# Optimization experiments

Measured on AMD Instinct MI355X. Metric: run time of the kernel, lower is better.

Reference implementation:

```python
import jax, jax.numpy as jnp
import numpy as np

N = 20000
IN_CH = 2048      # 64 * (768/24)
HID = 512
LAT = 128
KW = 24           # conv1d kernel == stride
COUT = 64
NEG_SLOPE = 0.2
BN_EPS = 1e-5


def gatv2(x, src, dst, Wl, bl, Wr, br, att, bias, n_nodes):
    # GATv2Conv (PyG semantics, 1 head): e_ij = att . leaky_relu(Wl x_j + Wr x_i)
    xl = x @ Wl + bl                      # [N, out] source-side features
    xr = x @ Wr + br                      # [N, out] target-side features
    e = jax.nn.leaky_relu(xl[src] + xr[dst], NEG_SLOPE) @ att   # [E]
    m = jax.ops.segment_max(e, dst, num_segments=n_nodes)       # per-target max
    a = jnp.exp(e - m[dst])
    s = jax.ops.segment_sum(a, dst, num_segments=n_nodes)
    alpha = a / (s[dst] + 1e-16)
    out = jax.ops.segment_sum(xl[src] * alpha[:, None], dst, num_segments=n_nodes)
    return out + bias


def setup_inputs() -> dict:
    key = jax.random.key(0)
    ks = jax.random.split(key, 16)
    x = jax.random.normal(ks[0], (N, 24, 32), dtype=jnp.float32)
    edge_index = jax.random.randint(ks[1], (2, 320000), 0, N, dtype=jnp.int32)
    sc = 0.02
    return {
        "x": x,
        "edge_index": edge_index,
        "conv_w": jax.random.normal(ks[2], (COUT, KW), dtype=jnp.float32) * sc,
        "conv_b": jnp.zeros((COUT,), dtype=jnp.float32),
        "W1l": jax.random.normal(ks[3], (IN_CH, HID), dtype=jnp.float32) * sc,
        "b1l": jnp.zeros((HID,), dtype=jnp.float32),
        "W1r": jax.random.normal(ks[4], (IN_CH, HID), dtype=jnp.float32) * sc,
        "b1r": jnp.zeros((HID,), dtype=jnp.float32),
        "att1": jax.random.normal(ks[5], (HID,), dtype=jnp.float32) * sc,
        "bias1": jnp.zeros((HID,), dtype=jnp.float32),
        "gamma": jnp.ones((HID,), dtype=jnp.float32),
        "beta": jnp.zeros((HID,), dtype=jnp.float32),
        "W2l": jax.random.normal(ks[6], (HID, LAT), dtype=jnp.float32) * sc,
        "b2l": jnp.zeros((LAT,), dtype=jnp.float32),
        "W2r": jax.random.normal(ks[7], (HID, LAT), dtype=jnp.float32) * sc,
        "b2r": jnp.zeros((LAT,), dtype=jnp.float32),
        "att2": jax.random.normal(ks[8], (LAT,), dtype=jnp.float32) * sc,
        "bias2": jnp.zeros((LAT,), dtype=jnp.float32),
    }


def reference(x, edge_index, conv_w, conv_b, W1l, b1l, W1r, b1r, att1, bias1,
              gamma, beta, W2l, b2l, W2r, b2r, att2, bias2):
    n = x.shape[0]
    # x.transpose(1,2).flatten(1): [N,24,32] -> [N,32,24] -> [N,768]
    flat = jnp.transpose(x, (0, 2, 1)).reshape(n, -1)
    # Conv1d(1,64,24,stride=24): kernel==stride => reshape into segments of 24
    segs = flat.reshape(n, -1, KW)                       # [N, 32, 24]
    conv = jnp.einsum("ntk,ok->not", segs, conv_w) + conv_b[None, :, None]  # [N,64,32]
    h = conv.reshape(n, -1)                              # [N, 2048] (channel-major like torch .view)

    # add self-loops (PyG GATv2Conv default add_self_loops=True)
    loops = jnp.arange(n, dtype=edge_index.dtype)
    src = jnp.concatenate([edge_index[0], loops])
    dst = jnp.concatenate([edge_index[1], loops])

    h = gatv2(h, src, dst, W1l, b1l, W1r, b1r, att1, bias1, n)
    h = jax.nn.relu(h)
    # BatchNorm1d in training mode: batch stats over nodes, biased variance
    mean = jnp.mean(h, axis=0)
    var = jnp.mean((h - mean) ** 2, axis=0)
    h = gamma * (h - mean) / jnp.sqrt(var + BN_EPS) + beta

    mu = gatv2(h, src, dst, W2l, b2l, W2r, b2r, att2, bias2, n)
    return mu
```

## Files before the change

### kernel.cpp

```cpp
#include <hip/hip_runtime.h>
#include <cstdint>
#include <cstddef>
#include <type_traits>

static constexpr int NN   = 20000;
static constexpr int MPAD = 20096;
static constexpr int ERAW = 320000;
static constexpr int ETOT = ERAW + NN;

typedef __attribute__((ext_vector_type(8))) short bf16x8;
typedef __attribute__((ext_vector_type(8))) unsigned short u16x8;
typedef __attribute__((ext_vector_type(4))) float f32x4;

__device__ __forceinline__ unsigned short f2bf(float f) {
  union { float f; unsigned u; } v; v.f = f;
  unsigned r = v.u + 0x7fffu + ((v.u >> 16) & 1u);
  return (unsigned short)(r >> 16);
}
__device__ __forceinline__ float bf2f(unsigned short u) {
  union { unsigned u; float f; } v; v.u = ((unsigned)u) << 16;
  return v.f;
}

__device__ __forceinline__ void gload_lds16(const void* g, void* l) {
  __builtin_amdgcn_global_load_lds(
      (const __attribute__((address_space(1))) unsigned int*)g,
      (__attribute__((address_space(3))) unsigned int*)l, 16, 0, 0);
}

__global__ __launch_bounds__(256) void zero_init_kernel(
    int* __restrict__ degp, float* __restrict__ stats, float* __restrict__ beff1, int n) {
  int i = blockIdx.x * 256 + threadIdx.x;
  if (i < n) degp[i] = 0;
  if (i < 1024) { stats[i] = 0.f; beff1[i] = 0.f; }
}

__global__ __launch_bounds__(256) void cast_x_kernel(
    const float* __restrict__ x, unsigned short* __restrict__ xb) {
  int i8 = blockIdx.x * 256 + threadIdx.x;
  size_t base = (size_t)i8 * 8;
  int row = i8 / 96;
  u16x8 o;
  if (row < NN) {
    float4 a = *(const float4*)&x[base];
    float4 b = *(const float4*)&x[base + 4];
    o[0] = f2bf(a.x); o[1] = f2bf(a.y); o[2] = f2bf(a.z); o[3] = f2bf(a.w);
    o[4] = f2bf(b.x); o[5] = f2bf(b.y); o[6] = f2bf(b.z); o[7] = f2bf(b.w);
  } else {
#pragma unroll
    for (int j = 0; j < 8; j++) o[j] = 0;
  }
  *(u16x8*)&xb[base] = o;
}

__global__ __launch_bounds__(256) void weff_kernel(
    const float* __restrict__ conv_w, const float* __restrict__ conv_b,
    const float* __restrict__ W1l, const float* __restrict__ b1l,
    const float* __restrict__ W1r, const float* __restrict__ b1r,
    unsigned short* __restrict__ wc1, float* __restrict__ beff1) {
  __shared__ float ws[64 * 24];
  int t = blockIdx.x;
  int tid = threadIdx.x;
  for (int i = tid; i < 64 * 24; i += 256) ws[i] = conv_w[i];
  __syncthreads();
  int c = blockIdx.y * 256 + tid;
  const float* W; const float* bb; int cl;
  if (c < 512) { W = W1l; bb = b1l; cl = c; } else { W = W1r; bb = b1r; cl = c - 512; }
  float acc[24];
#pragma unroll
  for (int k = 0; k < 24; k++) acc[k] = 0.f;
  float bacc = (t == 0) ? bb[cl] : 0.f;
  for (int o = 0; o < 64; o++) {
    float Wv = W[(size_t)(o * 32 + t) * 512 + cl];
    bacc += conv_b[o] * Wv;
#pragma unroll
    for (int k = 0; k < 24; k++) acc[k] += ws[o * 24 + k] * Wv;
  }
#pragma unroll
  for (int k = 0; k < 24; k++) wc1[(size_t)c * 768 + k * 32 + t] = f2bf(acc[k]);
  atomicAdd(&beff1[c], bacc);
}

__global__ __launch_bounds__(256) void bnscale_kernel(
    const float* __restrict__ stats, const float* __restrict__ gamma,
    const float* __restrict__ beta, float* __restrict__ scsh) {
  int k = blockIdx.x * 256 + threadIdx.x;
  float mean = stats[k] * (1.f / NN);
  float var = stats[512 + k] * (1.f / NN) - mean * mean;
  float rstd = rsqrtf(var + 1e-5f);
  float sc = gamma[k] * rstd;
  scsh[k] = sc;
  scsh[512 + k] = beta[k] - sc * mean;
}

__global__ __launch_bounds__(256) void w2fold_kernel(
    const float* __restrict__ scsh,
    const float* __restrict__ W2l, const float* __restrict__ b2l,
    const float* __restrict__ W2r, const float* __restrict__ b2r,
    unsigned short* __restrict__ wc2, float* __restrict__ beff2) {
  int c = blockIdx.x;
  const float* W; const float* bb; int cl;
  if (c < 128) { W = W2l; bb = b2l; cl = c; } else { W = W2r; bb = b2r; cl = c - 128; }
  int tid = threadIdx.x, lane = tid & 63, wid = tid >> 6;
  float part = 0.f;
#pragma unroll
  for (int j = 0; j < 2; j++) {
    int k = tid * 2 + j;
    float wv = W[(size_t)k * 128 + cl];
    wc2[(size_t)c * 512 + k] = f2bf(scsh[k] * wv);
    part += scsh[512 + k] * wv;
  }
#pragma unroll
  for (int d = 32; d; d >>= 1) part += __shfl_xor(part, d);
  __shared__ float wsum[4];
  if (lane == 0) wsum[wid] = part;
  __syncthreads();
  if (tid == 0) beff2[c] = bb[cl] + wsum[0] + wsum[1] + wsum[2] + wsum[3];
}

template <typename OutT>
__global__ __launch_bounds__(256, 5) void gemm_kernel(
    const unsigned short* __restrict__ A, const unsigned short* __restrict__ B,
    const float* __restrict__ bias0, const float* __restrict__ bias1,
    OutT* __restrict__ C0, OutT* __restrict__ C1,
    int M, int K, int NT, int nsplit, int swz) {
  __shared__ __align__(16) unsigned short As[128 * 64];
  __shared__ __align__(16) unsigned short Bs[128 * 64];
  int bid = blockIdx.x;
  if (swz) bid = (bid & 7) * (gridDim.x >> 3) + (bid >> 3);
  int tm = bid / NT, tn = bid % NT;
  int tid = threadIdx.x, wid = tid >> 6, lane = tid & 63;
  int wr = wid >> 1, wc = wid & 1;
  const unsigned short* gA = A + (size_t)(tm * 128) * K;
  const unsigned short* gB = B + (size_t)(tn * 128) * K;
  int srow = wid * 8 + (lane >> 3);
  int scol = ((lane & 7) ^ (lane >> 3)) * 8;

  f32x4 acc[4][4];
  f32x4 zero = {0.f, 0.f, 0.f, 0.f};
#pragma unroll
  for (int i = 0; i < 4; i++)
#pragma unroll
    for (int j = 0; j < 4; j++) acc[i][j] = zero;

  int KT = K >> 6;
  for (int kt = 0; kt < KT; ++kt) {
    if (kt) __syncthreads();
    {
      const unsigned short* a0 = gA + (size_t)srow * K + kt * 64 + scol;
      const unsigned short* b0 = gB + (size_t)srow * K + kt * 64 + scol;
#pragma unroll
      for (int i = 0; i < 4; i++)
        gload_lds16(a0 + (size_t)i * 32 * K, &As[i * 2048 + wid * 512]);
#pragma unroll
      for (int i = 0; i < 4; i++)
        gload_lds16(b0 + (size_t)i * 32 * K, &Bs[i * 2048 + wid * 512]);
    }
    asm volatile("s_waitcnt vmcnt(0)" ::: "memory");
    __syncthreads();
#pragma unroll
    for (int kk = 0; kk < 2; kk++) {
      int ko = kk * 32 + (lane >> 4) * 8;
      int kosw = ko ^ ((lane & 7) << 3);
      bf16x8 af[4], bfr[4];
#pragma unroll
      for (int mi = 0; mi < 4; mi++)
        af[mi] = *(const bf16x8*)&As[(wr * 64 + mi * 16 + (lane & 15)) * 64 + kosw];
#pragma unroll
      for (int ni = 0; ni < 4; ni++)
        bfr[ni] = *(const bf16x8*)&Bs[(wc * 64 + ni * 16 + (lane & 15)) * 64 + kosw];
#pragma unroll
      for (int mi = 0; mi < 4; mi++)
#pragma unroll
        for (int ni = 0; ni < 4; ni++)
          acc[mi][ni] = __builtin_amdgcn_mfma_f32_16x16x32_bf16(
              af[mi], bfr[ni], acc[mi][ni], 0, 0, 0);
    }
  }

  int ncol_tile = tn * 128;
  OutT* Cd; const float* bs; int col0;
  if (ncol_tile < nsplit) { Cd = C0; bs = bias0; col0 = ncol_tile; }
  else { Cd = C1; bs = bias1; col0 = ncol_tile - nsplit; }
#pragma unroll
  for (int mi = 0; mi < 4; mi++) {
    int rbase = tm * 128 + wr * 64 + mi * 16 + (lane >> 4) * 4;
#pragma unroll
    for (int ni = 0; ni < 4; ni++) {
      int c = col0 + wc * 64 + ni * 16 + (lane & 15);
      float bv = bs[c];
#pragma unroll
      for (int j = 0; j < 4; j++) {
        int r = rbase + j;
        if (r < M) {
          float v = acc[mi][ni][j] + bv;
          if constexpr (sizeof(OutT) == 2) Cd[(size_t)r * nsplit + c] = f2bf(v);
          else Cd[(size_t)r * nsplit + c] = v;
        }
      }
    }
  }
}

__global__ void hist_kernel(const int* __restrict__ dst, int* deg, int E) {
  int e = blockIdx.x * 256 + threadIdx.x;
  if (e < E) atomicAdd(&deg[dst[e]], 1);
}
__global__ __launch_bounds__(1024) void scan1_kernel(
    const int* __restrict__ deg, int* __restrict__ off, int* __restrict__ btot, int n) {
  __shared__ int wsum[16];
  int tid = threadIdx.x, lane = tid & 63, w = tid >> 6;
  int i = blockIdx.x * 1024 + tid;
  int v = (i < n) ? deg[i] + 1 : 0;
  int s = v;
#pragma unroll
  for (int d = 1; d < 64; d <<= 1) {
    int t = __shfl_up(s, d);
    if (lane >= d) s += t;
  }
  if (lane == 63) wsum[w] = s;
  __syncthreads();
  if (w == 0 && lane < 16) {
    int t = wsum[lane];
#pragma unroll
    for (int d = 1; d < 16; d <<= 1) {
      int u = __shfl_up(t, d);
      if (lane >= d) t += u;
    }
    wsum[lane] = t;
  }
  __syncthreads();
  int incl = (w ? wsum[w - 1] : 0) + s;
  if (i < n) off[i] = incl - v;
  if (tid == 1023) btot[blockIdx.x] = incl;
}
__global__ void scan2_kernel(const int* __restrict__ btot, int* __restrict__ gbase,
                             int* __restrict__ off, int nb, int n) {
  int lane = threadIdx.x;
  int v = lane < nb ? btot[lane] : 0;
  int s = v;
#pragma unroll
  for (int d = 1; d < 64; d <<= 1) {
    int t = __shfl_up(s, d);
    if (lane >= d) s += t;
  }
  if (lane < nb) gbase[lane] = s - v;
  if (lane == nb - 1) off[n] = s;
}
__global__ __launch_bounds__(1024) void scan3_kernel(
    int* __restrict__ off, int* __restrict__ cursor,
    const int* __restrict__ gbase, int* __restrict__ esrc, int n) {
  int i = blockIdx.x * 1024 + threadIdx.x;
  if (i < n) {
    int v = off[i] + gbase[blockIdx.x];
    off[i] = v;
    cursor[i] = v + 1;
    esrc[v] = i;
  }
}
__global__ void scatter_kernel(const int* __restrict__ src, const int* __restrict__ dst,
                               int* cursor, int* __restrict__ esrc, int E) {
  int e = blockIdx.x * 256 + threadIdx.x;
  if (e < E) {
    int pos = atomicAdd(&cursor[dst[e]], 1);
    esrc[pos] = src[e];
  }
}

template <int VPL, typename OutT>
__global__ __launch_bounds__(256) void gat_agg_kernel(
    const unsigned short* __restrict__ xl, const unsigned short* __restrict__ xr,
    const float* __restrict__ att, const float* __restrict__ bias,
    const int* __restrict__ off, const int* __restrict__ esrc,
    OutT* __restrict__ out, int n, int do_relu) {
  constexpr int C = VPL * 64;
  using RawT = std::conditional_t<VPL == 8, bf16x8, unsigned int>;
  int node = blockIdx.x * 4 + (threadIdx.x >> 6);
  int lane = threadIdx.x & 63;
  int base = lane * VPL;
  if (node >= n) {
#pragma unroll
    for (int v = 0; v < VPL; v++) out[(size_t)node * C + base + v] = OutT(0);
    return;
  }
  float xrv[VPL], attv[VPL];
#pragma unroll
  for (int v = 0; v < VPL; v++) {
    xrv[v] = bf2f(xr[(size_t)node * C + base + v]);
    attv[v] = att[base + v];
  }
  float s0 = 0.f, s1 = 0.f;
  float acc0[VPL], acc1[VPL];
#pragma unroll
  for (int v = 0; v < VPL; v++) { acc0[v] = 0.f; acc1[v] = 0.f; }
  int e0 = off[node], e1 = off[node + 1];
  int e = e0;
  for (; e + 1 < e1; e += 2) {
    RawT r0 = *(const RawT*)(xl + (size_t)esrc[e] * C + base);
    RawT r1 = *(const RawT*)(xl + (size_t)esrc[e + 1] * C + base);
    float x0[VPL], x1[VPL];
    if constexpr (VPL == 8) {
#pragma unroll
      for (int v = 0; v < 8; v++) { x0[v] = bf2f((unsigned short)r0[v]);
                                    x1[v] = bf2f((unsigned short)r1[v]); }
    } else {
      x0[0] = bf2f((unsigned short)(r0 & 0xffffu)); x0[1] = bf2f((unsigned short)(r0 >> 16));
      x1[0] = bf2f((unsigned short)(r1 & 0xffffu)); x1[1] = bf2f((unsigned short)(r1 >> 16));
    }
    float p0 = 0.f, p1 = 0.f;
#pragma unroll
    for (int v = 0; v < VPL; v++) {
      float t0 = x0[v] + xrv[v]; t0 = t0 > 0.f ? t0 : 0.2f * t0;
      float t1 = x1[v] + xrv[v]; t1 = t1 > 0.f ? t1 : 0.2f * t1;
      p0 += attv[v] * t0;
      p1 += attv[v] * t1;
    }
#pragma unroll
    for (int d2 = 32; d2; d2 >>= 1) { p0 += __shfl_xor(p0, d2); p1 += __shfl_xor(p1, d2); }
    float w0 = __expf(p0), w1 = __expf(p1);
    s0 += w0; s1 += w1;
#pragma unroll
    for (int v = 0; v < VPL; v++) { acc0[v] += w0 * x0[v]; acc1[v] += w1 * x1[v]; }
  }
  if (e < e1) {
    RawT r0 = *(const RawT*)(xl + (size_t)esrc[e] * C + base);
    float x0[VPL];
    if constexpr (VPL == 8) {
#pragma unroll
      for (int v = 0; v < 8; v++) x0[v] = bf2f((unsigned short)r0[v]);
    } else {
      x0[0] = bf2f((unsigned short)(r0 & 0xffffu)); x0[1] = bf2f((unsigned short)(r0 >> 16));
    }
    float p0 = 0.f;
#pragma unroll
    for (int v = 0; v < VPL; v++) {
      float t0 = x0[v] + xrv[v]; t0 = t0 > 0.f ? t0 : 0.2f * t0;
      p0 += attv[v] * t0;
    }
#pragma unroll
    for (int d2 = 32; d2; d2 >>= 1) p0 += __shfl_xor(p0, d2);
    float w0 = __expf(p0);
    s0 += w0;
#pragma unroll
    for (int v = 0; v < VPL; v++) acc0[v] += w0 * x0[v];
  }
  float inv = 1.f / (s0 + s1 + 1e-16f);
#pragma unroll
  for (int v = 0; v < VPL; v++) {
    float o = (acc0[v] + acc1[v]) * inv + bias[base + v];
    if (do_relu) o = fmaxf(o, 0.f);
    if constexpr (sizeof(OutT) == 2) out[(size_t)node * C + base + v] = f2bf(o);
    else out[(size_t)node * C + base + v] = o;
  }
}

__global__ __launch_bounds__(256) void bn_stats_kernel(
    const unsigned short* __restrict__ h1, float* __restrict__ stats, int n) {
  int tid = threadIdx.x;
  int c0 = tid * 2;
  int r0 = blockIdx.x * 128;
  int r1 = r0 + 128 < n ? r0 + 128 : n;
  float s0 = 0, q0 = 0, s1 = 0, q1 = 0;
  for (int r = r0; r < r1; ++r) {
    unsigned u = *(const unsigned*)&h1[(size_t)r * 512 + c0];
    float a = bf2f((unsigned short)(u & 0xffffu));
    float b = bf2f((unsigned short)(u >> 16));
    s0 += a; q0 += a * a; s1 += b; q1 += b * b;
  }
  atomicAdd(&stats[c0], s0);
  atomicAdd(&stats[c0 + 1], s1);
  atomicAdd(&stats[512 + c0], q0);
  atomicAdd(&stats[512 + c0 + 1], q1);
}

extern "C" void kernel_launch(void* const* d_in, const int* in_sizes, int n_in,
                              void* d_out, int out_size, void* d_ws, size_t ws_size,
                              hipStream_t stream) {
  (void)in_sizes; (void)n_in; (void)out_size; (void)ws_size;
  const float* x      = (const float*)d_in[0];
  const int*   ei     = (const int*)d_in[1];
  const float* conv_w = (const float*)d_in[2];
  const float* conv_b = (const float*)d_in[3];
  const float* W1l    = (const float*)d_in[4];
  const float* b1l    = (const float*)d_in[5];
  const float* W1r    = (const float*)d_in[6];
  const float* b1r    = (const float*)d_in[7];
  const float* att1   = (const float*)d_in[8];
  const float* bias1  = (const float*)d_in[9];
  const float* gamma  = (const float*)d_in[10];
  const float* beta   = (const float*)d_in[11];
  const float* W2l    = (const float*)d_in[12];
  const float* b2l    = (const float*)d_in[13];
  const float* W2r    = (const float*)d_in[14];
  const float* b2r    = (const float*)d_in[15];
  const float* att2   = (const float*)d_in[16];
  const float* bias2  = (const float*)d_in[17];

  char* ws = (char*)d_ws;
  size_t off = 0;
  auto alloc = [&](size_t bytes) {
    size_t r = off;
    off += (bytes + 255) & ~(size_t)255;
    return r;
  };
  size_t o_xb   = alloc((size_t)MPAD * 768 * 2);
  size_t o_wc1  = alloc((size_t)1024 * 768 * 2);
  size_t o_wc2  = alloc((size_t)256 * 512 * 2);
  size_t o_xl1  = alloc((size_t)NN * 512 * 2);
  size_t o_xr1  = alloc((size_t)NN * 512 * 2);
  size_t o_h1   = alloc((size_t)MPAD * 512 * 2);
  size_t o_xl2  = alloc((size_t)NN * 128 * 2);
  size_t o_xr2  = alloc((size_t)NN * 128 * 2);
  size_t o_off  = alloc((size_t)(NN + 1) * 4);
  size_t o_cur  = alloc((size_t)NN * 4);
  size_t o_deg  = alloc((size_t)NN * 4);
  size_t o_esrc = alloc((size_t)ETOT * 4);
  size_t o_stats = alloc((size_t)1024 * 4);
  size_t o_scsh  = alloc((size_t)1024 * 4);
  size_t o_beff1 = alloc((size_t)1024 * 4);
  size_t o_beff2 = alloc((size_t)256 * 4);
  size_t o_btot  = alloc((size_t)64 * 4);
  size_t o_gbase = alloc((size_t)64 * 4);

  unsigned short* xb  = (unsigned short*)(ws + o_xb);
  unsigned short* wc1 = (unsigned short*)(ws + o_wc1);
  unsigned short* wc2 = (unsigned short*)(ws + o_wc2);
  unsigned short* xl1 = (unsigned short*)(ws + o_xl1);
  unsigned short* xr1 = (unsigned short*)(ws + o_xr1);
  unsigned short* h1  = (unsigned short*)(ws + o_h1);
  unsigned short* xl2 = (unsigned short*)(ws + o_xl2);
  unsigned short* xr2 = (unsigned short*)(ws + o_xr2);
  int* offp  = (int*)(ws + o_off);
  int* curp  = (int*)(ws + o_cur);
  int* degp  = (int*)(ws + o_deg);
  int* esrc  = (int*)(ws + o_esrc);
  float* stats = (float*)(ws + o_stats);
  float* scsh  = (float*)(ws + o_scsh);
  float* beff1 = (float*)(ws + o_beff1);
  float* beff2 = (float*)(ws + o_beff2);
  int* btot  = (int*)(ws + o_btot);
  int* gbase = (int*)(ws + o_gbase);

  const int* src_raw = ei;
  const int* dst_raw = ei + ERAW;
  float* mu = (float*)d_out;

  zero_init_kernel<<<(NN + 255) / 256, 256, 0, stream>>>(degp, stats, beff1, NN);
  cast_x_kernel<<<(MPAD * 96) / 256, 256, 0, stream>>>(x, xb);
  weff_kernel<<<dim3(32, 4), 256, 0, stream>>>(conv_w, conv_b, W1l, b1l, W1r, b1r, wc1, beff1);

  hist_kernel<<<(ERAW + 255) / 256, 256, 0, stream>>>(dst_raw, degp, ERAW);
  const int NB = (NN + 1023) / 1024;
  scan1_kernel<<<NB, 1024, 0, stream>>>(degp, offp, btot, NN);
  scan2_kernel<<<1, 64, 0, stream>>>(btot, gbase, offp, NB, NN);
  scan3_kernel<<<NB, 1024, 0, stream>>>(offp, curp, gbase, esrc, NN);
  scatter_kernel<<<(ERAW + 255) / 256, 256, 0, stream>>>(src_raw, dst_raw, curp, esrc, ERAW);

  gemm_kernel<unsigned short><<<(MPAD / 128) * (1024 / 128), 256, 0, stream>>>(
      xb, wc1, beff1, beff1 + 512, xl1, xr1, NN, 768, 8, 512, 1);
  gat_agg_kernel<8, unsigned short><<<MPAD / 4, 256, 0, stream>>>(
      xl1, xr1, att1, bias1, offp, esrc, h1, NN, 1);

  bn_stats_kernel<<<(NN + 127) / 128, 256, 0, stream>>>(h1, stats, NN);
  bnscale_kernel<<<2, 256, 0, stream>>>(stats, gamma, beta, scsh);
  w2fold_kernel<<<256, 256, 0, stream>>>(scsh, W2l, b2l, W2r, b2r, wc2, beff2);

  gemm_kernel<unsigned short><<<(MPAD / 128) * (256 / 128), 256, 0, stream>>>(
      h1, wc2, beff2, beff2 + 128, xl2, xr2, NN, 512, 2, 128, 0);
  gat_agg_kernel<2, float><<<NN / 4, 256, 0, stream>>>(
      xl2, xr2, att2, bias2, offp, esrc, mu, NN, 0);
}
```

Before: 298.2 us.

## Fuse init and BN-scale kernels, unroll GAT aggregation by four edges

Folds the zero-init work into the cast kernel and the BN scale/shift computation into the weight-folding kernel, which removes two launches and the scratch buffer between them. The GAT aggregation loop now processes four edges per iteration, so four gathers are in flight together, and uses cheaper shift/mask bf16 conversions and fmax for leaky-relu. The weff kernel batches its weight loads four at a time. The larger unroll raises register pressure in the aggregation kernel.

```diff
diff --git a/kernel.cpp b/kernel.cpp
--- a/kernel.cpp
+++ b/kernel.cpp
@@ -28,16 +28,12 @@
       (__attribute__((address_space(3))) unsigned int*)l, 16, 0, 0);
 }
 
-__global__ __launch_bounds__(256) void zero_init_kernel(
-    int* __restrict__ degp, float* __restrict__ stats, float* __restrict__ beff1, int n) {
-  int i = blockIdx.x * 256 + threadIdx.x;
-  if (i < n) degp[i] = 0;
-  if (i < 1024) { stats[i] = 0.f; beff1[i] = 0.f; }
-}
-
 __global__ __launch_bounds__(256) void cast_x_kernel(
-    const float* __restrict__ x, unsigned short* __restrict__ xb) {
+    const float* __restrict__ x, unsigned short* __restrict__ xb,
+    int* __restrict__ degp, float* __restrict__ stats, float* __restrict__ beff1) {
   int i8 = blockIdx.x * 256 + threadIdx.x;
+  if (i8 < NN) degp[i8] = 0;
+  if (i8 < 1024) { stats[i8] = 0.f; beff1[i8] = 0.f; }
   size_t base = (size_t)i8 * 8;
   int row = i8 / 96;
   u16x8 o;
@@ -70,31 +66,25 @@
 #pragma unroll
   for (int k = 0; k < 24; k++) acc[k] = 0.f;
   float bacc = (t == 0) ? bb[cl] : 0.f;
-  for (int o = 0; o < 64; o++) {
-    float Wv = W[(size_t)(o * 32 + t) * 512 + cl];
-    bacc += conv_b[o] * Wv;
-#pragma unroll
-    for (int k = 0; k < 24; k++) acc[k] += ws[o * 24 + k] * Wv;
+  for (int o = 0; o < 64; o += 4) {
+    float Wv[4];
+#pragma unroll
+    for (int j = 0; j < 4; j++) Wv[j] = W[(size_t)((o + j) * 32 + t) * 512 + cl];
+#pragma unroll
+    for (int j = 0; j < 4; j++) {
+      bacc += conv_b[o + j] * Wv[j];
+#pragma unroll
+      for (int k = 0; k < 24; k++) acc[k] += ws[(o + j) * 24 + k] * Wv[j];
+    }
   }
 #pragma unroll
   for (int k = 0; k < 24; k++) wc1[(size_t)c * 768 + k * 32 + t] = f2bf(acc[k]);
   atomicAdd(&beff1[c], bacc);
 }
 
-__global__ __launch_bounds__(256) void bnscale_kernel(
+__global__ __launch_bounds__(256) void w2fold_kernel(
     const float* __restrict__ stats, const float* __restrict__ gamma,
-    const float* __restrict__ beta, float* __restrict__ scsh) {
-  int k = blockIdx.x * 256 + threadIdx.x;
-  float mean = stats[k] * (1.f / NN);
-  float var = stats[512 + k] * (1.f / NN) - mean * mean;
-  float rstd = rsqrtf(var + 1e-5f);
-  float sc = gamma[k] * rstd;
-  scsh[k] = sc;
-  scsh[512 + k] = beta[k] - sc * mean;
-}
-
-__global__ __launch_bounds__(256) void w2fold_kernel(
-    const float* __restrict__ scsh,
+    const float* __restrict__ beta,
     const float* __restrict__ W2l, const float* __restrict__ b2l,
     const float* __restrict__ W2r, const float* __restrict__ b2r,
     unsigned short* __restrict__ wc2, float* __restrict__ beff2) {
@@ -106,9 +96,14 @@
 #pragma unroll
   for (int j = 0; j < 2; j++) {
     int k = tid * 2 + j;
+    float mean = stats[k] * (1.f / NN);
+    float var = stats[512 + k] * (1.f / NN) - mean * mean;
+    float rstd = rsqrtf(var + 1e-5f);
+    float sc = gamma[k] * rstd;
+    float sh = beta[k] - sc * mean;
     float wv = W[(size_t)k * 128 + cl];
-    wc2[(size_t)c * 512 + k] = f2bf(scsh[k] * wv);
-    part += scsh[512 + k] * wv;
+    wc2[(size_t)c * 512 + k] = f2bf(sc * wv);
+    part += sh * wv;
   }
 #pragma unroll
   for (int d = 32; d; d >>= 1) part += __shfl_xor(part, d);
@@ -274,7 +269,7 @@
     const int* __restrict__ off, const int* __restrict__ esrc,
     OutT* __restrict__ out, int n, int do_relu) {
   constexpr int C = VPL * 64;
-  using RawT = std::conditional_t<VPL == 8, bf16x8, unsigned int>;
+  using RawT = std::conditional_t<VPL == 8, uint4, unsigned int>;
   int node = blockIdx.x * 4 + (threadIdx.x >> 6);
   int lane = threadIdx.x & 63;
   int base = lane * VPL;
@@ -289,54 +284,61 @@
     xrv[v] = bf2f(xr[(size_t)node * C + base + v]);
     attv[v] = att[base + v];
   }
+  auto cvt = [](RawT r, float* xv) {
+    if constexpr (VPL == 8) {
+      unsigned u[4] = {r.x, r.y, r.z, r.w};
+#pragma unroll
+      for (int i = 0; i < 4; i++) {
+        xv[2 * i]     = __uint_as_float(u[i] << 16);
+        xv[2 * i + 1] = __uint_as_float(u[i] & 0xffff0000u);
+      }
+    } else {
+      xv[0] = __uint_as_float(r << 16);
+      xv[1] = __uint_as_float(r & 0xffff0000u);
+    }
+  };
+  auto score = [&](const float* xv) {
+    float p = 0.f;
+#pragma unroll
+    for (int v = 0; v < VPL; v++) {
+      float t = xv[v] + xrv[v];
+      p += attv[v] * fmaxf(t, 0.2f * t);
+    }
+    return p;
+  };
   float s0 = 0.f, s1 = 0.f;
   float acc0[VPL], acc1[VPL];
 #pragma unroll
   for (int v = 0; v < VPL; v++) { acc0[v] = 0.f; acc1[v] = 0.f; }
   int e0 = off[node], e1 = off[node + 1];
   int e = e0;
-  for (; e + 1 < e1; e += 2) {
-    RawT r0 = *(const RawT*)(xl + (size_t)esrc[e] * C + base);
-    RawT r1 = *(const RawT*)(xl + (size_t)esrc[e + 1] * C + base);
-    float x0[VPL], x1[VPL];
-    if constexpr (VPL == 8) {
-#pragma unroll
-      for (int v = 0; v < 8; v++) { x0[v] = bf2f((unsigned short)r0[v]);
-                                    x1[v] = bf2f((unsigned short)r1[v]); }
-    } else {
-      x0[0] = bf2f((unsigned short)(r0 & 0xffffu)); x0[1] = bf2f((unsigned short)(r0 >> 16));
-      x1[0] = bf2f((unsigned short)(r1 & 0xffffu)); x1[1] = bf2f((unsigned short)(r1 >> 16));
-    }
-    float p0 = 0.f, p1 = 0.f;
+  for (; e + 3 < e1; e += 4) {
+    int s0i = esrc[e], s1i = esrc[e + 1], s2i = esrc[e + 2], s3i = esrc[e + 3];
+    RawT r0 = *(const RawT*)(xl + (size_t)s0i * C + base);
+    RawT r1 = *(const RawT*)(xl + (size_t)s1i * C + base);
+    RawT r2 = *(const RawT*)(xl + (size_t)s2i * C + base);
+    RawT r3 = *(const RawT*)(xl + (size_t)s3i * C + base);
+    float x0[VPL], x1[VPL], x2[VPL], x3[VPL];
+    cvt(r0, x0); cvt(r1, x1); cvt(r2, x2); cvt(r3, x3);
+    float p0 = score(x0), p1 = score(x1), p2 = score(x2), p3 = score(x3);
+#pragma unroll
+    for (int d2 = 32; d2; d2 >>= 1) {
+      p0 += __shfl_xor(p0, d2); p1 += __shfl_xor(p1, d2);
+      p2 += __shfl_xor(p2, d2); p3 += __shfl_xor(p3, d2);
+    }
+    float w0 = __expf(p0), w1 = __expf(p1), w2 = __expf(p2), w3 = __expf(p3);
+    s0 += w0 + w2; s1 += w1 + w3;
 #pragma unroll
     for (int v = 0; v < VPL; v++) {
-      float t0 = x0[v] + xrv[v]; t0 = t0 > 0.f ? t0 : 0.2f * t0;
-      float t1 = x1[v] + xrv[v]; t1 = t1 > 0.f ? t1 : 0.2f * t1;
-      p0 += attv[v] * t0;
-      p1 += attv[v] * t1;
-    }
-#pragma unroll
-    for (int d2 = 32; d2; d2 >>= 1) { p0 += __shfl_xor(p0, d2); p1 += __shfl_xor(p1, d2); }
-    float w0 = __expf(p0), w1 = __expf(p1);
-    s0 += w0; s1 += w1;
-#pragma unroll
-    for (int v = 0; v < VPL; v++) { acc0[v] += w0 * x0[v]; acc1[v] += w1 * x1[v]; }
-  }
-  if (e < e1) {
+      acc0[v] += w0 * x0[v] + w2 * x2[v];
+      acc1[v] += w1 * x1[v] + w3 * x3[v];
+    }
+  }
+  for (; e < e1; ++e) {
     RawT r0 = *(const RawT*)(xl + (size_t)esrc[e] * C + base);
     float x0[VPL];
-    if constexpr (VPL == 8) {
-#pragma unroll
-      for (int v = 0; v < 8; v++) x0[v] = bf2f((unsigned short)r0[v]);
-    } else {
-      x0[0] = bf2f((unsigned short)(r0 & 0xffffu)); x0[1] = bf2f((unsigned short)(r0 >> 16));
-    }
-    float p0 = 0.f;
-#pragma unroll
-    for (int v = 0; v < VPL; v++) {
-      float t0 = x0[v] + xrv[v]; t0 = t0 > 0.f ? t0 : 0.2f * t0;
-      p0 += attv[v] * t0;
-    }
+    cvt(r0, x0);
+    float p0 = score(x0);
 #pragma unroll
     for (int d2 = 32; d2; d2 >>= 1) p0 += __shfl_xor(p0, d2);
     float w0 = __expf(p0);
@@ -363,8 +365,8 @@
   float s0 = 0, q0 = 0, s1 = 0, q1 = 0;
   for (int r = r0; r < r1; ++r) {
     unsigned u = *(const unsigned*)&h1[(size_t)r * 512 + c0];
-    float a = bf2f((unsigned short)(u & 0xffffu));
-    float b = bf2f((unsigned short)(u >> 16));
+    float a = __uint_as_float(u << 16);
+    float b = __uint_as_float(u & 0xffff0000u);
     s0 += a; q0 += a * a; s1 += b; q1 += b * b;
   }
   atomicAdd(&stats[c0], s0);
@@ -416,7 +418,6 @@
   size_t o_deg  = alloc((size_t)NN * 4);
   size_t o_esrc = alloc((size_t)ETOT * 4);
   size_t o_stats = alloc((size_t)1024 * 4);
-  size_t o_scsh  = alloc((size_t)1024 * 4);
   size_t o_beff1 = alloc((size_t)1024 * 4);
   size_t o_beff2 = alloc((size_t)256 * 4);
   size_t o_btot  = alloc((size_t)64 * 4);
@@ -435,7 +436,6 @@
   int* degp  = (int*)(ws + o_deg);
   int* esrc  = (int*)(ws + o_esrc);
   float* stats = (float*)(ws + o_stats);
-  float* scsh  = (float*)(ws + o_scsh);
   float* beff1 = (float*)(ws + o_beff1);
   float* beff2 = (float*)(ws + o_beff2);
   int* btot  = (int*)(ws + o_btot);
@@ -445,8 +445,7 @@
   const int* dst_raw = ei + ERAW;
   float* mu = (float*)d_out;
 
-  zero_init_kernel<<<(NN + 255) / 256, 256, 0, stream>>>(degp, stats, beff1, NN);
-  cast_x_kernel<<<(MPAD * 96) / 256, 256, 0, stream>>>(x, xb);
+  cast_x_kernel<<<(MPAD * 96) / 256, 256, 0, stream>>>(x, xb, degp, stats, beff1);
   weff_kernel<<<dim3(32, 4), 256, 0, stream>>>(conv_w, conv_b, W1l, b1l, W1r, b1r, wc1, beff1);
 
   hist_kernel<<<(ERAW + 255) / 256, 256, 0, stream>>>(dst_raw, degp, ERAW);
@@ -462,8 +461,7 @@
       xl1, xr1, att1, bias1, offp, esrc, h1, NN, 1);
 
   bn_stats_kernel<<<(NN + 127) / 128, 256, 0, stream>>>(h1, stats, NN);
-  bnscale_kernel<<<2, 256, 0, stream>>>(stats, gamma, beta, scsh);
-  w2fold_kernel<<<256, 256, 0, stream>>>(scsh, W2l, b2l, W2r, b2r, wc2, beff2);
+  w2fold_kernel<<<256, 256, 0, stream>>>(stats, gamma, beta, W2l, b2l, W2r, b2r, wc2, beff2);
 
   gemm_kernel<unsigned short><<<(MPAD / 128) * (256 / 128), 256, 0, stream>>>(
       h1, wc2, beff2, beff2 + 128, xl2, xr2, NN, 512, 2, 128, 0);
```

New measurement: 282.3 us. -5.3%, faster.
